# Kernel tuning notes

Hardware: AMD Instinct MI355X
Metric: run time of the kernel (lower is better)

Reference implementation:

```python
import jax, jax.numpy as jnp
import numpy as np

# module config (init_kwargs)
PATCH = 256
STRIDE = 128
B, C, H, W = 2, 3, 1024, 1024
PH = (H - (PATCH - 1) - 1) // STRIDE + 1  # 7
PW = (W - (PATCH - 1) - 1) // STRIDE + 1  # 7


def setup_inputs() -> dict:
    key = jax.random.key(0)
    x = jax.random.normal(key, (PH * PW, B, C, PATCH, PATCH), dtype=jnp.float32)
    return {"x": x}


def reference(x) -> jnp.ndarray:
    # Max-fold overlapping patches back into the full image.
    # Equivalent to the torch code's (ph*pw, b, c, h, w) -inf buffer + max over
    # dim 0, but folded in place: scatter-max each patch into a single buffer.
    out = jnp.full((B, C, H, W), -jnp.inf, dtype=x.dtype)
    for i in range(PH):
        for j in range(PW):
            idx = PW * i + j
            hs, ws = i * STRIDE, j * STRIDE
            region = out[:, :, hs:hs + PATCH, ws:ws + PATCH]
            out = out.at[:, :, hs:hs + PATCH, ws:ws + PATCH].set(
                jnp.maximum(region, x[idx]))
    return out
```

## Files before the change

### kernel.cpp

```cpp
#include <hip/hip_runtime.h>

#define PATCH   256
#define STRIDEP 128
#define Bn      2
#define Cn      3
#define Hn      1024
#define Wn      1024
#define PHn     7
#define PWn     7

typedef float v4f __attribute__((ext_vector_type(4)));

#define KCHUNK  3
#define NBLK    2048
#define CHUNK_STRIDE (NBLK * 256)

__global__ __launch_bounds__(256) void unpatch_max_kernel(
    const float* __restrict__ x, float* __restrict__ out)
{
    const int gid = blockIdx.x * blockDim.x + threadIdx.x;

    #pragma unroll
    for (int k = 0; k < KCHUNK; ++k) {
        const int cid = gid + k * CHUNK_STRIDE;
        const int w4   = cid & 255;
        const int rest = cid >> 8;
        const int h    = rest & (Hn - 1);
        const int bc   = rest >> 10;
        const int w    = w4 << 2;

        const int hi = h >> 7;
        const int i1 = hi < PHn ? hi : (PHn - 1);
        const int i0 = hi > 0 ? hi - 1 : 0;
        const int wi = w >> 7;
        const int j1 = wi < PWn ? wi : (PWn - 1);
        const int j0 = wi > 0 ? wi - 1 : 0;

        v4f m = (v4f){-INFINITY, -INFINITY, -INFINITY, -INFINITY};

        #pragma unroll 2
        for (int i = i0; i <= i1; ++i) {
            const int ph = h - i * STRIDEP;
            #pragma unroll 2
            for (int j = j0; j <= j1; ++j) {
                const int pw  = w - j * STRIDEP;
                const int idx = i * PWn + j;
                const float* p = x +
                    ((size_t)(idx * (Bn * Cn) + bc) * PATCH + ph) * PATCH + pw;
                m = __builtin_elementwise_max(m, *reinterpret_cast<const v4f*>(p));
            }
        }

        __builtin_nontemporal_store(
            m, reinterpret_cast<v4f*>(out + (size_t)cid * 4));
    }
}

extern "C" void kernel_launch(void* const* d_in, const int* in_sizes, int n_in,
                              void* d_out, int out_size, void* d_ws, size_t ws_size,
                              hipStream_t stream)
{
    const float* x = (const float*)d_in[0];
    float* out = (float*)d_out;
    unpatch_max_kernel<<<NBLK, 256, 0, stream>>>(x, out);
}
```

Measured before the change: 21.64 us.

## Remap threads to wave-uniform 128-column bands with specialized overlap branches

```diff
diff --git a/kernel.cpp b/kernel.cpp
--- a/kernel.cpp
+++ b/kernel.cpp
@@ -1,58 +1,79 @@
 #include <hip/hip_runtime.h>
 
-#define PATCH   256
-#define STRIDEP 128
-#define Bn      2
-#define Cn      3
-#define Hn      1024
-#define Wn      1024
-#define PHn     7
-#define PWn     7
 
 typedef float v4f __attribute__((ext_vector_type(4)));
 
-#define KCHUNK  3
-#define NBLK    2048
-#define CHUNK_STRIDE (NBLK * 256)
+#define KCHUNK 3
+#define NBLK   2048
 
 __global__ __launch_bounds__(256) void unpatch_max_kernel(
     const float* __restrict__ x, float* __restrict__ out)
 {
-    const int gid = blockIdx.x * blockDim.x + threadIdx.x;
+    const int tid  = blockIdx.x * 256 + threadIdx.x;
+    const int lane = tid & 63;
+    const int colq = lane & 31;
+    const int rpar = lane >> 5;
 
-    #pragma unroll
-    for (int k = 0; k < KCHUNK; ++k) {
-        const int cid = gid + k * CHUNK_STRIDE;
-        const int w4   = cid & 255;
-        const int rest = cid >> 8;
-        const int h    = rest & (Hn - 1);
-        const int bc   = rest >> 10;
-        const int w    = w4 << 2;
+    const int wid  = __builtin_amdgcn_readfirstlane(tid >> 6);
+    const int band = wid & 7;
+    const int row2 = (wid >> 3) & 511;
+    const int bc0  = wid >> 12;
 
-        const int hi = h >> 7;
-        const int i1 = hi < PHn ? hi : (PHn - 1);
-        const int i0 = hi > 0 ? hi - 1 : 0;
-        const int wi = w >> 7;
-        const int j1 = wi < PWn ? wi : (PWn - 1);
-        const int j0 = wi > 0 ? wi - 1 : 0;
+    const int hi = row2 >> 6;
+    const int i0 = hi - (hi > 0);
+    const int j0 = band - (band > 0);
+    const bool i2 = (hi > 0) & (hi < 7);
+    const bool j2 = (band > 0) & (band < 7);
 
-        v4f m = (v4f){-INFINITY, -INFINITY, -INFINITY, -INFINITY};
+    const int h = row2 * 2 + rpar;
+    const int w = band * 128 + colq * 4;
 
-        #pragma unroll 2
-        for (int i = i0; i <= i1; ++i) {
-            const int ph = h - i * STRIDEP;
-            #pragma unroll 2
-            for (int j = j0; j <= j1; ++j) {
-                const int pw  = w - j * STRIDEP;
-                const int idx = i * PWn + j;
-                const float* p = x +
-                    ((size_t)(idx * (Bn * Cn) + bc) * PATCH + ph) * PATCH + pw;
-                m = __builtin_elementwise_max(m, *reinterpret_cast<const v4f*>(p));
-            }
+    const size_t DI = (size_t)7 * 6 * 65536 - 128 * 256;
+    const size_t DJ = (size_t)6 * 65536 - 128;
+    const size_t DB = (size_t)2 * 65536;
+    const size_t DO = (size_t)2 * 1024 * 1024;
+
+    const float* p = x + (size_t)((i0 * 7 + j0) * 6 + bc0) * 65536
+                       + (size_t)(h - i0 * 128) * 256 + (w - j0 * 128);
+    float* o = out + (size_t)(bc0 * 1024 + h) * 1024 + w;
+
+    if (i2 & j2) {
+        #pragma unroll
+        for (int k = 0; k < KCHUNK; ++k) {
+            const float* pk = p + (size_t)k * DB;
+            const v4f a = *reinterpret_cast<const v4f*>(pk);
+            const v4f b = *reinterpret_cast<const v4f*>(pk + DJ);
+            const v4f c = *reinterpret_cast<const v4f*>(pk + DI);
+            const v4f d = *reinterpret_cast<const v4f*>(pk + DI + DJ);
+            const v4f m = __builtin_elementwise_max(
+                __builtin_elementwise_max(a, b),
+                __builtin_elementwise_max(c, d));
+            __builtin_nontemporal_store(m, reinterpret_cast<v4f*>(o + k * DO));
         }
-
-        __builtin_nontemporal_store(
-            m, reinterpret_cast<v4f*>(out + (size_t)cid * 4));
+    } else if (i2) {
+        #pragma unroll
+        for (int k = 0; k < KCHUNK; ++k) {
+            const float* pk = p + (size_t)k * DB;
+            const v4f a = *reinterpret_cast<const v4f*>(pk);
+            const v4f c = *reinterpret_cast<const v4f*>(pk + DI);
+            __builtin_nontemporal_store(__builtin_elementwise_max(a, c),
+                                        reinterpret_cast<v4f*>(o + k * DO));
+        }
+    } else if (j2) {
+        #pragma unroll
+        for (int k = 0; k < KCHUNK; ++k) {
+            const float* pk = p + (size_t)k * DB;
+            const v4f a = *reinterpret_cast<const v4f*>(pk);
+            const v4f b = *reinterpret_cast<const v4f*>(pk + DJ);
+            __builtin_nontemporal_store(__builtin_elementwise_max(a, b),
+                                        reinterpret_cast<v4f*>(o + k * DO));
+        }
+    } else {
+        #pragma unroll
+        for (int k = 0; k < KCHUNK; ++k) {
+            const v4f a = *reinterpret_cast<const v4f*>(p + (size_t)k * DB);
+            __builtin_nontemporal_store(a, reinterpret_cast<v4f*>(o + k * DO));
+        }
     }
 }
 
```

After: 23.44 us, median of 2. 8.3% more time.

## Compute four output rows per thread with 64-thread blocks

Applied to the files above, without the earlier changes.

```diff
diff --git a/kernel.cpp b/kernel.cpp
--- a/kernel.cpp
+++ b/kernel.cpp
@@ -1,59 +1,54 @@
 #include <hip/hip_runtime.h>
 
-#define PATCH   256
-#define STRIDEP 128
-#define Bn      2
-#define Cn      3
-#define Hn      1024
-#define Wn      1024
-#define PHn     7
-#define PWn     7
 
 typedef float v4f __attribute__((ext_vector_type(4)));
 
-#define KCHUNK  3
-#define NBLK    2048
-#define CHUNK_STRIDE (NBLK * 256)
-
-__global__ __launch_bounds__(256) void unpatch_max_kernel(
+__global__ __launch_bounds__(64) void unpatch_max_kernel(
     const float* __restrict__ x, float* __restrict__ out)
 {
-    const int gid = blockIdx.x * blockDim.x + threadIdx.x;
+    const int tid = blockIdx.x * 64 + threadIdx.x;
+    const int w4   = tid & 255;
+    const int rest = tid >> 8;
+    const int rq   = rest & 255;
+    const int bc   = rest >> 8;
 
-    #pragma unroll
-    for (int k = 0; k < KCHUNK; ++k) {
-        const int cid = gid + k * CHUNK_STRIDE;
-        const int w4   = cid & 255;
-        const int rest = cid >> 8;
-        const int h    = rest & (Hn - 1);
-        const int bc   = rest >> 10;
-        const int w    = w4 << 2;
+    const int h0 = rq << 2;
+    const int w  = w4 << 2;
 
-        const int hi = h >> 7;
-        const int i1 = hi < PHn ? hi : (PHn - 1);
-        const int i0 = hi > 0 ? hi - 1 : 0;
-        const int wi = w >> 7;
-        const int j1 = wi < PWn ? wi : (PWn - 1);
-        const int j0 = wi > 0 ? wi - 1 : 0;
+    const int hi = h0 >> 7;
+    const int i1 = hi < 7 ? hi : 6;
+    const int i0 = hi > 0 ? hi - 1 : 0;
+    const int wi = w >> 7;
+    const int j1 = wi < 7 ? wi : 6;
+    const int j0 = wi > 0 ? wi - 1 : 0;
 
-        v4f m = (v4f){-INFINITY, -INFINITY, -INFINITY, -INFINITY};
+    v4f m0 = (v4f){-INFINITY, -INFINITY, -INFINITY, -INFINITY};
+    v4f m1 = m0, m2 = m0, m3 = m0;
 
+    #pragma unroll 2
+    for (int i = i0; i <= i1; ++i) {
+        const int ph0 = h0 - i * 128;
         #pragma unroll 2
-        for (int i = i0; i <= i1; ++i) {
-            const int ph = h - i * STRIDEP;
-            #pragma unroll 2
-            for (int j = j0; j <= j1; ++j) {
-                const int pw  = w - j * STRIDEP;
-                const int idx = i * PWn + j;
-                const float* p = x +
-                    ((size_t)(idx * (Bn * Cn) + bc) * PATCH + ph) * PATCH + pw;
-                m = __builtin_elementwise_max(m, *reinterpret_cast<const v4f*>(p));
-            }
+        for (int j = j0; j <= j1; ++j) {
+            const int pw  = w - j * 128;
+            const float* p = x +
+                ((size_t)((i * 7 + j) * 6 + bc) << 16) + (size_t)ph0 * 256 + pw;
+            const v4f a0 = *reinterpret_cast<const v4f*>(p);
+            const v4f a1 = *reinterpret_cast<const v4f*>(p + 256);
+            const v4f a2 = *reinterpret_cast<const v4f*>(p + 512);
+            const v4f a3 = *reinterpret_cast<const v4f*>(p + 768);
+            m0 = __builtin_elementwise_max(m0, a0);
+            m1 = __builtin_elementwise_max(m1, a1);
+            m2 = __builtin_elementwise_max(m2, a2);
+            m3 = __builtin_elementwise_max(m3, a3);
         }
+    }
 
-        __builtin_nontemporal_store(
-            m, reinterpret_cast<v4f*>(out + (size_t)cid * 4));
-    }
+    float* o = out + ((size_t)bc << 20) + (size_t)h0 * 1024 + w;
+    __builtin_nontemporal_store(m0, reinterpret_cast<v4f*>(o));
+    __builtin_nontemporal_store(m1, reinterpret_cast<v4f*>(o + 1024));
+    __builtin_nontemporal_store(m2, reinterpret_cast<v4f*>(o + 2048));
+    __builtin_nontemporal_store(m3, reinterpret_cast<v4f*>(o + 3072));
 }
 
 extern "C" void kernel_launch(void* const* d_in, const int* in_sizes, int n_in,
@@ -62,5 +57,6 @@
 {
     const float* x = (const float*)d_in[0];
     float* out = (float*)d_out;
-    unpatch_max_kernel<<<NBLK, 256, 0, stream>>>(x, out);
+
+    unpatch_max_kernel<<<6144, 64, 0, stream>>>(x, out);
 }
```

After: 21.06 us. 2.7% less time.
